# Kernel optimization log

Hardware: AMD Instinct MI355X
Metric: run time of the kernel (lower is better)

Reference implementation:

```python
import jax, jax.numpy as jnp
import numpy as np

N = 50000
E = 1600000
NFEAT = 128
NHID = 128
NEG_SLOPE_ATT = 0.2   # GATConv attention leaky_relu
NEG_SLOPE_ACT = 0.01  # F.leaky_relu default between layers


def setup_inputs() -> dict:
    key = jax.random.key(0)
    ks = jax.random.split(key, 12)
    x = jax.random.normal(ks[0], (N, NFEAT), dtype=jnp.float32)
    edge_index = jax.random.randint(ks[1], (2, E), 0, N, dtype=jnp.int64)
    s1 = 1.0 / np.sqrt(NFEAT)
    s2 = 1.0 / np.sqrt(NHID)
    return {
        "x": x,
        "edge_index": edge_index,
        "W1": jax.random.normal(ks[2], (NFEAT, NHID), dtype=jnp.float32) * s1,
        "att_src1": jax.random.normal(ks[3], (NHID,), dtype=jnp.float32) * s2,
        "att_dst1": jax.random.normal(ks[4], (NHID,), dtype=jnp.float32) * s2,
        "b1": jnp.zeros((NHID,), dtype=jnp.float32),
        "W2": jax.random.normal(ks[5], (NHID, NHID), dtype=jnp.float32) * s2,
        "att_src2": jax.random.normal(ks[6], (NHID,), dtype=jnp.float32) * s2,
        "att_dst2": jax.random.normal(ks[7], (NHID,), dtype=jnp.float32) * s2,
        "b2": jnp.zeros((NHID,), dtype=jnp.float32),
    }


def _gat_conv(x, src, dst, W, a_src, a_dst, b):
    # single-head GATConv (PyG defaults), self-loops already in src/dst
    h = x @ W                                  # [N, nhid]
    alpha_s = h @ a_src                        # [N]
    alpha_d = h @ a_dst                        # [N]
    e = jax.nn.leaky_relu(alpha_s[src] + alpha_d[dst], NEG_SLOPE_ATT)  # [E']
    # softmax over incoming edges per destination node
    m = jax.ops.segment_max(e, dst, num_segments=N)
    e = jnp.exp(e - m[dst])
    denom = jax.ops.segment_sum(e, dst, num_segments=N)
    alpha = e / (denom[dst] + 1e-16)
    out = jax.ops.segment_sum(h[src] * alpha[:, None], dst, num_segments=N)
    return out + b


def reference(x, edge_index, W1, att_src1, att_dst1, b1, W2, att_src2, att_dst2, b2):
    loops = jnp.arange(N, dtype=edge_index.dtype)
    src = jnp.concatenate([edge_index[0], loops])  # add_self_loops=True
    dst = jnp.concatenate([edge_index[1], loops])
    h = _gat_conv(x, src, dst, W1, att_src1, att_dst1, b1)
    h = jax.nn.leaky_relu(h, NEG_SLOPE_ACT)
    out = _gat_conv(h, src, dst, W2, att_src2, att_dst2, b2)
    return out
```

## Files before the change

kernel.cpp:

```cpp
#include <hip/hip_runtime.h>
#include <hip/hip_fp16.h>

constexpr int N  = 50000;
constexpr int E  = 1600000;
constexpr int ET = E + N;
constexpr int NF = 128;
constexpr int BSH = 128;
constexpr int NB = (N + BSH - 1) / BSH;
constexpr int CAP = 8192;
constexpr int EPB  = 8192;
constexpr int NBLK = (ET + EPB - 1) / EPB;
constexpr int SCAPW = 128;

typedef _Float16 half8 __attribute__((ext_vector_type(8)));
typedef float    f32x4 __attribute__((ext_vector_type(4)));

__global__ __launch_bounds__(256) void k_init_packw(
    int* __restrict__ bcur,
    const float* __restrict__ W1, const float* __restrict__ W2,
    __half* __restrict__ P1, __half* __restrict__ P2) {
    int tid = blockIdx.x * 256 + threadIdx.x;
    if (tid < NB) bcur[tid] = tid * CAP;
    if (tid >= 2 * NF * NF) return;
    int which = tid >> 14;
    int id = tid & (NF * NF - 1);
    int k = id >> 7, n = id & 127;
    const float* W = which ? W2 : W1;
    __half* P = which ? P2 : P1;
    int ks = k >> 5, r = k & 31, ct = n >> 4;
    int lane = ((r >> 3) << 4) | (n & 15);
    int j = r & 7;
    P[((ks * 8 + ct) * 64 + lane) * 8 + j] = __float2half_rn(W[k * NF + n]);
}

__global__ __launch_bounds__(1024) void k_binscatter(const int* __restrict__ ei,
                                                     int* __restrict__ bcur,
                                                     int* __restrict__ packed) {
    __shared__ int h[NB], lcur[NB], garr[NB];
    int t = threadIdx.x;
    for (int i = t; i < NB; i += 1024) h[i] = 0;
    __syncthreads();
    int base = blockIdx.x * EPB;
    int pk[EPB / 1024];
    int bk[EPB / 1024];
#pragma unroll
    for (int k = 0; k < EPB / 1024; ++k) {
        int i = base + k * 1024 + t;
        if (i < ET) {
            int s, d;
            if (i < E) { s = ei[i]; d = ei[E + i]; } else { s = i - E; d = i - E; }
            bk[k] = d >> 7;
            pk[k] = s | ((d & (BSH - 1)) << 16);
            atomicAdd(&h[bk[k]], 1);
        } else bk[k] = -1;
    }
    __syncthreads();
    for (int i = t; i < NB; i += 1024) {
        lcur[i] = 0;
        garr[i] = h[i] ? atomicAdd(&bcur[i], h[i]) : 0;
    }
    __syncthreads();
#pragma unroll
    for (int k = 0; k < EPB / 1024; ++k) {
        if (bk[k] >= 0) {
            int p = garr[bk[k]] + atomicAdd(&lcur[bk[k]], 1);
            packed[p] = pk[k];
        }
    }
}

__global__ __launch_bounds__(512) void k_csr(const int* __restrict__ packed,
                                             const int* __restrict__ bcur,
                                             int* __restrict__ offB, int* __restrict__ offE,
                                             unsigned short* __restrict__ srcs) {
    int b = blockIdx.x;
    int t = threadIdx.x;
    int s0 = b * CAP;
    int n = bcur[b] - s0;
    __shared__ int buf[CAP];
    __shared__ int h[BSH], bas[BSH], lcur[BSH];
    for (int i = t; i < n; i += 512) buf[i] = packed[s0 + i];
    if (t < BSH) { h[t] = 0; lcur[t] = 0; }
    __syncthreads();
    for (int i = t; i < n; i += 512)
        atomicAdd(&h[(buf[i] >> 16) & (BSH - 1)], 1);
    __syncthreads();
    if (t < 64) {
        int v0 = h[2 * t], v1 = h[2 * t + 1];
        int pair = v0 + v1, x = pair;
#pragma unroll
        for (int o = 1; o < 64; o <<= 1) {
            int y = __shfl_up(x, o);
            if (t >= o) x += y;
        }
        int e0 = s0 + x - pair;
        int e1 = e0 + v0;
        bas[2 * t] = e0; bas[2 * t + 1] = e1;
        int d = b * BSH + 2 * t;
        if (d < N)     { offB[d] = e0;     offE[d] = e1; }
        if (d + 1 < N) { offB[d + 1] = e1; offE[d + 1] = s0 + x; }
    }
    __syncthreads();
    for (int i = t; i < n; i += 512) {
        int p = buf[i];
        int dl = (p >> 16) & (BSH - 1);
        int pos = bas[dl] + atomicAdd(&lcur[dl], 1);
        srcs[pos] = (unsigned short)(p & 0xFFFF);
    }
}

template <typename AT>
__global__ __launch_bounds__(256) void k_gemm_mfma(
    const AT* __restrict__ A, const __half* __restrict__ Wpk,
    const float* __restrict__ asv, const float* __restrict__ adv,
    __half* __restrict__ H16, float* __restrict__ AS, float* __restrict__ AD) {
    int t = threadIdx.x;
    int wave = t >> 6, lane = t & 63;
    int base = blockIdx.x * 64 + wave * 16;

    int row_a = base + (lane & 15);
    if (row_a >= N) row_a = N - 1;
    const AT* Arow = A + (size_t)row_a * NF;
    const half8* BP = (const half8*)Wpk;

    f32x4 acc[8] = {};
#pragma unroll
    for (int ks = 0; ks < 4; ++ks) {
        int eo = (ks * 4 + (lane >> 4)) * 8;
        half8 a;
        if constexpr (sizeof(AT) == 4) {
            float4 u = *(const float4*)(Arow + eo);
            float4 v = *(const float4*)(Arow + eo + 4);
            a[0] = (_Float16)u.x; a[1] = (_Float16)u.y; a[2] = (_Float16)u.z; a[3] = (_Float16)u.w;
            a[4] = (_Float16)v.x; a[5] = (_Float16)v.y; a[6] = (_Float16)v.z; a[7] = (_Float16)v.w;
        } else {
            a = ((const half8*)Arow)[ks * 4 + (lane >> 4)];
        }
#pragma unroll
        for (int ct = 0; ct < 8; ++ct) {
            half8 b = BP[(ks * 8 + ct) * 64 + lane];
            acc[ct] = __builtin_amdgcn_mfma_f32_16x16x32_f16(a, b, acc[ct], 0, 0, 0);
        }
    }

    int colb = lane & 15;
    int rowq = base + (lane >> 4) * 4;
    float ps[4] = {0.f, 0.f, 0.f, 0.f};
    float pd[4] = {0.f, 0.f, 0.f, 0.f};
#pragma unroll
    for (int ct = 0; ct < 8; ++ct) {
        int col = ct * 16 + colb;
        float av = asv[col], dv = adv[col];
#pragma unroll
        for (int r = 0; r < 4; ++r) {
            float h = acc[ct][r];
            if (rowq + r < N) H16[(size_t)(rowq + r) * NF + col] = __float2half_rn(h);
            ps[r] = fmaf(h, av, ps[r]);
            pd[r] = fmaf(h, dv, pd[r]);
        }
    }
#pragma unroll
    for (int r = 0; r < 4; ++r) {
#pragma unroll
        for (int o = 1; o <= 8; o <<= 1) {
            ps[r] += __shfl_xor(ps[r], o);
            pd[r] += __shfl_xor(pd[r], o);
        }
    }
    if (colb == 0) {
#pragma unroll
        for (int r = 0; r < 4; ++r) {
            if (rowq + r < N) { AS[rowq + r] = ps[r]; AD[rowq + r] = pd[r]; }
        }
    }
}

template <typename OUTT, int ACT>
__global__ __launch_bounds__(256) void k_aggregate(
    const __half* __restrict__ H16, const float* __restrict__ AS, const float* __restrict__ AD,
    const int* __restrict__ offB, const int* __restrict__ offE,
    const unsigned short* __restrict__ srcs,
    const float* __restrict__ bias, OUTT* __restrict__ OUT) {
    int wave = threadIdx.x >> 6, lane = threadIdx.x & 63;
    int d = blockIdx.x * 4 + wave;

    __shared__ float ssv[4][SCAPW];
    __shared__ unsigned short ssrc[4][SCAPW];

    int beg = offB[d], deg = offE[d] - beg;
    float ad = AD[d];

    float ls = 0.f;
    for (int i = lane; i < deg; i += 64) {
        int s = srcs[beg + i];
        float sv = AS[s] + ad;
        sv = (sv > 0.f) ? sv : 0.2f * sv;
        float e = __expf(fminf(sv, 60.f));
        if (i < SCAPW) { ssv[wave][i] = e; ssrc[wave][i] = (unsigned short)s; }
        ls += e;
    }
#pragma unroll
    for (int o = 1; o <= 32; o <<= 1) ls += __shfl_xor(ls, o);
    float inv = 1.f / (ls + 1e-16f);

    int tx = lane & 15, u = lane >> 4;
    float acc[8] = {0.f, 0.f, 0.f, 0.f, 0.f, 0.f, 0.f, 0.f};
    for (int j0 = 0; j0 < deg; j0 += 8) {
        int i0 = j0 + u, i1 = j0 + 4 + u;
        float e0 = 0.f, e1 = 0.f;
        int s0 = 0, s1 = 0;
        bool v0 = i0 < deg, v1 = i1 < deg;
        if (v0) {
            if (i0 < SCAPW) { e0 = ssv[wave][i0]; s0 = ssrc[wave][i0]; }
            else {
                s0 = srcs[beg + i0];
                float sv = AS[s0] + ad;
                sv = (sv > 0.f) ? sv : 0.2f * sv;
                e0 = __expf(fminf(sv, 60.f));
            }
        }
        if (v1) {
            if (i1 < SCAPW) { e1 = ssv[wave][i1]; s1 = ssrc[wave][i1]; }
            else {
                s1 = srcs[beg + i1];
                float sv = AS[s1] + ad;
                sv = (sv > 0.f) ? sv : 0.2f * sv;
                e1 = __expf(fminf(sv, 60.f));
            }
        }
        union { float4 f; __half2 h[4]; } va, vb;
        if (v0) va.f = *reinterpret_cast<const float4*>(H16 + (size_t)s0 * NF + tx * 8);
        if (v1) vb.f = *reinterpret_cast<const float4*>(H16 + (size_t)s1 * NF + tx * 8);
        if (v0) {
            float2 f0 = __half22float2(va.h[0]);
            float2 f1 = __half22float2(va.h[1]);
            float2 f2 = __half22float2(va.h[2]);
            float2 f3 = __half22float2(va.h[3]);
            acc[0] = fmaf(e0, f0.x, acc[0]); acc[1] = fmaf(e0, f0.y, acc[1]);
            acc[2] = fmaf(e0, f1.x, acc[2]); acc[3] = fmaf(e0, f1.y, acc[3]);
            acc[4] = fmaf(e0, f2.x, acc[4]); acc[5] = fmaf(e0, f2.y, acc[5]);
            acc[6] = fmaf(e0, f3.x, acc[6]); acc[7] = fmaf(e0, f3.y, acc[7]);
        }
        if (v1) {
            float2 f0 = __half22float2(vb.h[0]);
            float2 f1 = __half22float2(vb.h[1]);
            float2 f2 = __half22float2(vb.h[2]);
            float2 f3 = __half22float2(vb.h[3]);
            acc[0] = fmaf(e1, f0.x, acc[0]); acc[1] = fmaf(e1, f0.y, acc[1]);
            acc[2] = fmaf(e1, f1.x, acc[2]); acc[3] = fmaf(e1, f1.y, acc[3]);
            acc[4] = fmaf(e1, f2.x, acc[4]); acc[5] = fmaf(e1, f2.y, acc[5]);
            acc[6] = fmaf(e1, f3.x, acc[6]); acc[7] = fmaf(e1, f3.y, acc[7]);
        }
    }
#pragma unroll
    for (int o = 16; o <= 32; o <<= 1) {
#pragma unroll
        for (int i = 0; i < 8; ++i) acc[i] += __shfl_xor(acc[i], o);
    }
    if (lane < 16) {
        float o8[8];
#pragma unroll
        for (int i = 0; i < 8; ++i) {
            float v = acc[i] * inv + bias[tx * 8 + i];
            o8[i] = (ACT && v < 0.f) ? 0.01f * v : v;
        }
        if constexpr (sizeof(OUTT) == 2) {
            union { __half2 h[4]; float4 f; } pk;
            pk.h[0] = __floats2half2_rn(o8[0], o8[1]);
            pk.h[1] = __floats2half2_rn(o8[2], o8[3]);
            pk.h[2] = __floats2half2_rn(o8[4], o8[5]);
            pk.h[3] = __floats2half2_rn(o8[6], o8[7]);
            ((float4*)OUT)[(size_t)d * 16 + tx] = pk.f;
        } else {
            float4 w0 = {o8[0], o8[1], o8[2], o8[3]};
            float4 w1 = {o8[4], o8[5], o8[6], o8[7]};
            ((float4*)OUT)[(size_t)d * 32 + tx * 2]     = w0;
            ((float4*)OUT)[(size_t)d * 32 + tx * 2 + 1] = w1;
        }
    }
}

extern "C" void kernel_launch(void* const* d_in, const int* in_sizes, int n_in,
                              void* d_out, int out_size, void* d_ws, size_t ws_size,
                              hipStream_t stream) {
    const float* x   = (const float*)d_in[0];
    const int*   ei  = (const int*)d_in[1];
    const float* W1  = (const float*)d_in[2];
    const float* as1 = (const float*)d_in[3];
    const float* ad1 = (const float*)d_in[4];
    const float* b1  = (const float*)d_in[5];
    const float* W2  = (const float*)d_in[6];
    const float* as2 = (const float*)d_in[7];
    const float* ad2 = (const float*)d_in[8];
    const float* b2  = (const float*)d_in[9];
    float* out = (float*)d_out;

    char* p = (char*)d_ws;
    auto alloc = [&](size_t bytes) { char* r = p; p += (bytes + 255) & ~size_t(255); return (void*)r; };
    int* bcur  = (int*)alloc(sizeof(int) * NB);
    int* offB  = (int*)alloc(sizeof(int) * N);
    int* offE  = (int*)alloc(sizeof(int) * N);
    unsigned short* srcs = (unsigned short*)alloc(sizeof(unsigned short) * (size_t)NB * CAP);
    __half* H16   = (__half*)alloc(sizeof(__half) * (size_t)N * NF);
    __half* HMID16= (__half*)alloc(sizeof(__half) * (size_t)N * NF);
    __half* Wpk1  = (__half*)alloc(sizeof(__half) * NF * NF);
    __half* Wpk2  = (__half*)alloc(sizeof(__half) * NF * NF);
    float* AS  = (float*)alloc(sizeof(float) * N);
    float* AD  = (float*)alloc(sizeof(float) * N);
    int* packed = (int*)alloc(sizeof(int) * (size_t)NB * CAP);

    k_init_packw<<<(2 * NF * NF + 255) / 256, 256, 0, stream>>>(bcur, W1, W2, Wpk1, Wpk2);
    k_binscatter<<<NBLK, 1024, 0, stream>>>(ei, bcur, packed);
    k_csr<<<NB, 512, 0, stream>>>(packed, bcur, offB, offE, srcs);

    k_gemm_mfma<float><<<(N + 63) / 64, 256, 0, stream>>>(x, Wpk1, as1, ad1, H16, AS, AD);
    k_aggregate<__half, 1><<<N / 4, 256, 0, stream>>>(H16, AS, AD, offB, offE, srcs, b1, HMID16);
    k_gemm_mfma<__half><<<(N + 63) / 64, 256, 0, stream>>>(HMID16, Wpk2, as2, ad2, H16, AS, AD);
    k_aggregate<float, 0><<<N / 4, 256, 0, stream>>>(H16, AS, AD, offB, offE, srcs, b2, out);
}
```

Before: 178.7 us.

## Fuse weight packing into binscatter and CSR build with layer-1 GEMM

Weight packing now runs as extra blocks of the edge bin-scatter kernel, and bucket cursors are zeroed with a memset instead of an init kernel. The CSR build and the layer-1 GEMM are merged into one launch with interleaved blocks, since the two are independent. The goal is fewer kernel launches and letting independent work run concurrently. The cost is a shared 512-thread block shape and full LDS allocation for GEMM blocks, which may lower occupancy.

```diff
diff --git a/kernel.cpp b/kernel.cpp
--- a/kernel.cpp
+++ b/kernel.cpp
@@ -10,34 +10,33 @@
 constexpr int CAP = 8192;
 constexpr int EPB  = 8192;
 constexpr int NBLK = (ET + EPB - 1) / EPB;
+constexpr int PACKW_BLKS = (2 * NF * NF + 1023) / 1024;
+constexpr int GEMM1_BLKS = (N + 127) / 128;
 constexpr int SCAPW = 128;
 
 typedef _Float16 half8 __attribute__((ext_vector_type(8)));
 typedef float    f32x4 __attribute__((ext_vector_type(4)));
 
-__global__ __launch_bounds__(256) void k_init_packw(
-    int* __restrict__ bcur,
+__global__ __launch_bounds__(1024) void k_scatter_packw(
+    const int* __restrict__ ei, int* __restrict__ bcur, int* __restrict__ packed,
     const float* __restrict__ W1, const float* __restrict__ W2,
     __half* __restrict__ P1, __half* __restrict__ P2) {
-    int tid = blockIdx.x * 256 + threadIdx.x;
-    if (tid < NB) bcur[tid] = tid * CAP;
-    if (tid >= 2 * NF * NF) return;
-    int which = tid >> 14;
-    int id = tid & (NF * NF - 1);
-    int k = id >> 7, n = id & 127;
-    const float* W = which ? W2 : W1;
-    __half* P = which ? P2 : P1;
-    int ks = k >> 5, r = k & 31, ct = n >> 4;
-    int lane = ((r >> 3) << 4) | (n & 15);
-    int j = r & 7;
-    P[((ks * 8 + ct) * 64 + lane) * 8 + j] = __float2half_rn(W[k * NF + n]);
-}
-
-__global__ __launch_bounds__(1024) void k_binscatter(const int* __restrict__ ei,
-                                                     int* __restrict__ bcur,
-                                                     int* __restrict__ packed) {
+    int t = threadIdx.x;
+    if (blockIdx.x >= NBLK) {
+        int tid = (blockIdx.x - NBLK) * 1024 + t;
+        if (tid >= 2 * NF * NF) return;
+        int which = tid >> 14;
+        int id = tid & (NF * NF - 1);
+        int k = id >> 7, n = id & 127;
+        const float* W = which ? W2 : W1;
+        __half* P = which ? P2 : P1;
+        int ks = k >> 5, r = k & 31, ct = n >> 4;
+        int lane = ((r >> 3) << 4) | (n & 15);
+        int j = r & 7;
+        P[((ks * 8 + ct) * 64 + lane) * 8 + j] = __float2half_rn(W[k * NF + n]);
+        return;
+    }
     __shared__ int h[NB], lcur[NB], garr[NB];
-    int t = threadIdx.x;
     for (int i = t; i < NB; i += 1024) h[i] = 0;
     __syncthreads();
     int base = blockIdx.x * EPB;
@@ -57,7 +56,7 @@
     __syncthreads();
     for (int i = t; i < NB; i += 1024) {
         lcur[i] = 0;
-        garr[i] = h[i] ? atomicAdd(&bcur[i], h[i]) : 0;
+        garr[i] = i * CAP + (h[i] ? atomicAdd(&bcur[i], h[i]) : 0);
     }
     __syncthreads();
 #pragma unroll
@@ -69,59 +68,15 @@
     }
 }
 
-__global__ __launch_bounds__(512) void k_csr(const int* __restrict__ packed,
-                                             const int* __restrict__ bcur,
-                                             int* __restrict__ offB, int* __restrict__ offE,
-                                             unsigned short* __restrict__ srcs) {
-    int b = blockIdx.x;
-    int t = threadIdx.x;
-    int s0 = b * CAP;
-    int n = bcur[b] - s0;
-    __shared__ int buf[CAP];
-    __shared__ int h[BSH], bas[BSH], lcur[BSH];
-    for (int i = t; i < n; i += 512) buf[i] = packed[s0 + i];
-    if (t < BSH) { h[t] = 0; lcur[t] = 0; }
-    __syncthreads();
-    for (int i = t; i < n; i += 512)
-        atomicAdd(&h[(buf[i] >> 16) & (BSH - 1)], 1);
-    __syncthreads();
-    if (t < 64) {
-        int v0 = h[2 * t], v1 = h[2 * t + 1];
-        int pair = v0 + v1, x = pair;
-#pragma unroll
-        for (int o = 1; o < 64; o <<= 1) {
-            int y = __shfl_up(x, o);
-            if (t >= o) x += y;
-        }
-        int e0 = s0 + x - pair;
-        int e1 = e0 + v0;
-        bas[2 * t] = e0; bas[2 * t + 1] = e1;
-        int d = b * BSH + 2 * t;
-        if (d < N)     { offB[d] = e0;     offE[d] = e1; }
-        if (d + 1 < N) { offB[d + 1] = e1; offE[d + 1] = s0 + x; }
-    }
-    __syncthreads();
-    for (int i = t; i < n; i += 512) {
-        int p = buf[i];
-        int dl = (p >> 16) & (BSH - 1);
-        int pos = bas[dl] + atomicAdd(&lcur[dl], 1);
-        srcs[pos] = (unsigned short)(p & 0xFFFF);
-    }
-}
-
 template <typename AT>
-__global__ __launch_bounds__(256) void k_gemm_mfma(
-    const AT* __restrict__ A, const __half* __restrict__ Wpk,
+__device__ __forceinline__ void gemm_rows16(
+    const AT* __restrict__ A, const half8* __restrict__ BP,
     const float* __restrict__ asv, const float* __restrict__ adv,
-    __half* __restrict__ H16, float* __restrict__ AS, float* __restrict__ AD) {
-    int t = threadIdx.x;
-    int wave = t >> 6, lane = t & 63;
-    int base = blockIdx.x * 64 + wave * 16;
-
+    __half* __restrict__ H16, float* __restrict__ AS, float* __restrict__ AD,
+    int base, int lane) {
     int row_a = base + (lane & 15);
     if (row_a >= N) row_a = N - 1;
     const AT* Arow = A + (size_t)row_a * NF;
-    const half8* BP = (const half8*)Wpk;
 
     f32x4 acc[8] = {};
 #pragma unroll
@@ -153,10 +108,10 @@
         float av = asv[col], dv = adv[col];
 #pragma unroll
         for (int r = 0; r < 4; ++r) {
-            float h = acc[ct][r];
-            if (rowq + r < N) H16[(size_t)(rowq + r) * NF + col] = __float2half_rn(h);
-            ps[r] = fmaf(h, av, ps[r]);
-            pd[r] = fmaf(h, dv, pd[r]);
+            float hv = acc[ct][r];
+            if (rowq + r < N) H16[(size_t)(rowq + r) * NF + col] = __float2half_rn(hv);
+            ps[r] = fmaf(hv, av, ps[r]);
+            pd[r] = fmaf(hv, dv, pd[r]);
         }
     }
 #pragma unroll
@@ -173,6 +128,65 @@
             if (rowq + r < N) { AS[rowq + r] = ps[r]; AD[rowq + r] = pd[r]; }
         }
     }
+}
+
+__global__ __launch_bounds__(512) void k_csr_gemm1(
+    const int* __restrict__ packed, const int* __restrict__ bcur,
+    int* __restrict__ offB, int* __restrict__ offE, unsigned short* __restrict__ srcs,
+    const float* __restrict__ X, const __half* __restrict__ Wpk,
+    const float* __restrict__ asv, const float* __restrict__ adv,
+    __half* __restrict__ H16, float* __restrict__ AS, float* __restrict__ AD) {
+    int t = threadIdx.x;
+    if ((blockIdx.x & 1) == 0) {
+        int blk = blockIdx.x >> 1;
+        int wave = t >> 6, lane = t & 63;
+        int base = blk * 128 + wave * 16;
+        gemm_rows16<float>(X, (const half8*)Wpk, asv, adv, H16, AS, AD, base, lane);
+        return;
+    }
+    int b = blockIdx.x >> 1;
+    int s0 = b * CAP;
+    int n = bcur[b];
+    __shared__ int buf[CAP];
+    __shared__ int h[BSH], bas[BSH], lcur[BSH];
+    for (int i = t; i < n; i += 512) buf[i] = packed[s0 + i];
+    if (t < BSH) { h[t] = 0; lcur[t] = 0; }
+    __syncthreads();
+    for (int i = t; i < n; i += 512)
+        atomicAdd(&h[(buf[i] >> 16) & (BSH - 1)], 1);
+    __syncthreads();
+    if (t < 64) {
+        int v0 = h[2 * t], v1 = h[2 * t + 1];
+        int pair = v0 + v1, x = pair;
+#pragma unroll
+        for (int o = 1; o < 64; o <<= 1) {
+            int y = __shfl_up(x, o);
+            if (t >= o) x += y;
+        }
+        int e0 = s0 + x - pair;
+        int e1 = e0 + v0;
+        bas[2 * t] = e0; bas[2 * t + 1] = e1;
+        int d = b * BSH + 2 * t;
+        if (d < N)     { offB[d] = e0;     offE[d] = e1; }
+        if (d + 1 < N) { offB[d + 1] = e1; offE[d + 1] = s0 + x; }
+    }
+    __syncthreads();
+    for (int i = t; i < n; i += 512) {
+        int p = buf[i];
+        int dl = (p >> 16) & (BSH - 1);
+        int pos = bas[dl] + atomicAdd(&lcur[dl], 1);
+        srcs[pos] = (unsigned short)(p & 0xFFFF);
+    }
+}
+
+__global__ __launch_bounds__(256) void k_gemm_mfma2(
+    const __half* __restrict__ A, const __half* __restrict__ Wpk,
+    const float* __restrict__ asv, const float* __restrict__ adv,
+    __half* __restrict__ H16, float* __restrict__ AS, float* __restrict__ AD) {
+    int t = threadIdx.x;
+    int wave = t >> 6, lane = t & 63;
+    int base = blockIdx.x * 64 + wave * 16;
+    gemm_rows16<__half>(A, (const half8*)Wpk, asv, adv, H16, AS, AD, base, lane);
 }
 
 template <typename OUTT, int ACT>
@@ -309,12 +323,11 @@
     float* AD  = (float*)alloc(sizeof(float) * N);
     int* packed = (int*)alloc(sizeof(int) * (size_t)NB * CAP);
 
-    k_init_packw<<<(2 * NF * NF + 255) / 256, 256, 0, stream>>>(bcur, W1, W2, Wpk1, Wpk2);
-    k_binscatter<<<NBLK, 1024, 0, stream>>>(ei, bcur, packed);
-    k_csr<<<NB, 512, 0, stream>>>(packed, bcur, offB, offE, srcs);
-
-    k_gemm_mfma<float><<<(N + 63) / 64, 256, 0, stream>>>(x, Wpk1, as1, ad1, H16, AS, AD);
+    hipMemsetAsync(bcur, 0, sizeof(int) * NB, stream);
+    k_scatter_packw<<<NBLK + PACKW_BLKS, 1024, 0, stream>>>(ei, bcur, packed, W1, W2, Wpk1, Wpk2);
+    k_csr_gemm1<<<2 * GEMM1_BLKS, 512, 0, stream>>>(packed, bcur, offB, offE, srcs,
+                                                    x, Wpk1, as1, ad1, H16, AS, AD);
     k_aggregate<__half, 1><<<N / 4, 256, 0, stream>>>(H16, AS, AD, offB, offE, srcs, b1, HMID16);
-    k_gemm_mfma<__half><<<(N + 63) / 64, 256, 0, stream>>>(HMID16, Wpk2, as2, ad2, H16, AS, AD);
+    k_gemm_mfma2<<<(N + 63) / 64, 256, 0, stream>>>(HMID16, Wpk2, as2, ad2, H16, AS, AD);
     k_aggregate<float, 0><<<N / 4, 256, 0, stream>>>(H16, AS, AD, offB, offE, srcs, b2, out);
 }
```

New measurement: 178.2 us. About the same (-0.3%).
